# Kernel optimization log

Hardware: AMD Instinct MI355X
Metric: run time of the kernel (lower is better)

Reference implementation:

```python
import jax, jax.numpy as jnp
import numpy as np

N, L, H, D = 2, 4096, 12, 64
HD = H * D

def setup_inputs() -> dict:
    key = jax.random.key(0)
    ks = jax.random.split(key, 5)
    s = 1.0 / np.sqrt(HD)  # keep projections well-scaled
    return {
        "x": jax.random.normal(ks[0], (N, L, HD), dtype=jnp.float32),
        "Wq": jax.random.normal(ks[1], (HD, HD), dtype=jnp.float32) * s,
        "bq": jnp.zeros((HD,), dtype=jnp.float32),
        "Wk": jax.random.normal(ks[2], (HD, HD), dtype=jnp.float32) * s,
        "bk": jnp.zeros((HD,), dtype=jnp.float32),
        "Wv": jax.random.normal(ks[3], (HD, HD), dtype=jnp.float32) * s,
        "bv": jnp.zeros((HD,), dtype=jnp.float32),
        "Wo": jax.random.normal(ks[4], (HD, HD), dtype=jnp.float32) * s,
        "bo": jnp.zeros((HD,), dtype=jnp.float32),
        "train": 0,
    }

def reference(x, Wq, bq, Wk, bk, Wv, bv, Wo, bo, train):
    n, l, hd = x.shape
    h, d = H, D
    # QKV projections (hk.Linear: x @ W + b), reshape to (n, l, h, d)
    q = (x @ Wq + bq).reshape(n, l, h, d)
    k = (x @ Wk + bk).reshape(n, l, h, d)
    v = (x @ Wv + bv).reshape(n, l, h, d)
    # scores: (n, q, k, h), scaled by sqrt(key_size)
    qkt = jnp.einsum('nqhd,nkhd->nqkh', q, k) / jnp.sqrt(jnp.float32(d))
    attn = jax.nn.softmax(qkt, axis=2)
    # eval mode: dropout_rate is 0.0, so dropout is identity
    o = jnp.einsum('nqkh,nkhd->nqhd', attn, v).reshape(n, l, hd)
    return o @ Wo + bo
```

## Files before the change

### kernel.cpp

```cpp
#include <hip/hip_runtime.h>

#define NN 2
#define LL 4096
#define HH 12
#define DD 64
#define HD_ 768
#define M_TOT (NN * LL)

typedef __bf16 bf16_t;
typedef _Float16 f16_t;
typedef __bf16 bf16x8 __attribute__((ext_vector_type(8)));
typedef __bf16 bf16x4 __attribute__((ext_vector_type(4)));
typedef _Float16 f16x2 __attribute__((ext_vector_type(2)));
typedef _Float16 f16x4 __attribute__((ext_vector_type(4)));
typedef _Float16 f16x8 __attribute__((ext_vector_type(8)));
typedef float floatx4 __attribute__((ext_vector_type(4)));

#define QSCALE 0.1803368801111f

__device__ __forceinline__ void async_load16(const bf16_t* g, bf16_t* l) {
    __builtin_amdgcn_global_load_lds(
        (const __attribute__((address_space(1))) unsigned int*)(g),
        (__attribute__((address_space(3))) unsigned int*)(l),
        16, 0, 0);
}

__device__ __forceinline__ f16x2 pkrtz(float a, float b) {
    return __builtin_bit_cast(f16x2, __builtin_amdgcn_cvt_pkrtz(a, b));
}

__global__ void cvt_kernel(const float* __restrict__ src, bf16_t* __restrict__ dst, int n4) {
    int i = blockIdx.x * blockDim.x + threadIdx.x;
    if (i < n4) {
        const float4 v = ((const float4*)src)[i];
        bf16_t* d = dst + (size_t)i * 4;
        d[0] = (bf16_t)v.x; d[1] = (bf16_t)v.y; d[2] = (bf16_t)v.z; d[3] = (bf16_t)v.w;
    }
}

struct WtArgs { const float* W[4]; bf16_t* Wt[4]; };
__global__ void cvt_wt_kernel(WtArgs a) {
    const int z = blockIdx.z;
    int id = blockIdx.x * 256 + threadIdx.x;
    int k = id / HD_;
    int n = id % HD_;
    a.Wt[z][(size_t)n * HD_ + k] = (bf16_t)a.W[z][id];
}

__device__ __forceinline__ void gemm_tile64(
    const bf16_t* __restrict__ A, const bf16_t* __restrict__ Bt,
    bf16_t* As, bf16_t* Bs, int m0, int n0, floatx4 (&acc)[2][2])
{
    const int tid  = threadIdx.x;
    const int lane = tid & 63;
    const int quad = lane >> 4, l16 = lane & 15;
    const int wave = tid >> 6;
    const int wm = wave >> 1, wn = wave & 1;
    const int lrow = tid >> 2;
    const int lcol = (tid & 3) * 16;

    for (int kt = 0; kt < HD_; kt += 64) {
        __syncthreads();
        {
            const bf16_t* ga = A + (size_t)(m0 + lrow) * HD_ + kt + lcol;
            *(bf16x8*)&As[lrow * 72 + lcol]     = *(const bf16x8*)ga;
            *(bf16x8*)&As[lrow * 72 + lcol + 8] = *(const bf16x8*)(ga + 8);
            const bf16_t* gb = Bt + (size_t)(n0 + lrow) * HD_ + kt + lcol;
            *(bf16x8*)&Bs[lrow * 72 + lcol]     = *(const bf16x8*)gb;
            *(bf16x8*)&Bs[lrow * 72 + lcol + 8] = *(const bf16x8*)(gb + 8);
        }
        __syncthreads();
        for (int ks = 0; ks < 2; ++ks) {
            bf16x8 af[2], bfr[2];
            af[0]  = *(const bf16x8*)&As[(wm * 32 + l16) * 72 + ks * 32 + quad * 8];
            af[1]  = *(const bf16x8*)&As[(wm * 32 + 16 + l16) * 72 + ks * 32 + quad * 8];
            bfr[0] = *(const bf16x8*)&Bs[(wn * 32 + l16) * 72 + ks * 32 + quad * 8];
            bfr[1] = *(const bf16x8*)&Bs[(wn * 32 + 16 + l16) * 72 + ks * 32 + quad * 8];
            for (int mi = 0; mi < 2; ++mi)
                for (int ni = 0; ni < 2; ++ni)
                    acc[mi][ni] = __builtin_amdgcn_mfma_f32_16x16x32_bf16(
                        af[mi], bfr[ni], acc[mi][ni], 0, 0, 0);
        }
    }
}

struct QKVArgs {
    const bf16_t* Bt[3];
    const float* bias[3];
    void* out[3];
};
__global__ __launch_bounds__(256) void gemm_qkv_kernel(const bf16_t* __restrict__ A, QKVArgs p)
{
    __shared__ __align__(16) bf16_t As[64 * 72];
    __shared__ __align__(16) bf16_t Bs[64 * 72];
    const int z = blockIdx.z;
    const int m0 = blockIdx.y * 64, n0 = blockIdx.x * 64;

    floatx4 acc[2][2] = {};
    gemm_tile64(A, p.Bt[z], As, Bs, m0, n0, acc);

    const int tid  = threadIdx.x;
    const int lane = tid & 63;
    const int quad = lane >> 4, l16 = lane & 15;
    const int wave = tid >> 6;
    const int wm = wave >> 1, wn = wave & 1;
    const float scale = (z == 0) ? QSCALE : 1.0f;
    const float* bias = p.bias[z];

    for (int ni = 0; ni < 2; ++ni) {
        const int col = n0 + wn * 32 + ni * 16 + l16;
        const float bv = bias[col];
        const int h = col >> 6, d = col & 63;
        for (int mi = 0; mi < 2; ++mi) {
            for (int r = 0; r < 4; ++r) {
                const int row = m0 + wm * 32 + mi * 16 + quad * 4 + r;
                const float val = (acc[mi][ni][r] + bv) * scale;
                const int nn = row >> 12, l = row & 4095;
                if (z == 2)
                    ((f16_t*)p.out[2])[(((size_t)nn * HH + h) * DD + d) * LL + l] = (f16_t)val;
                else
                    ((bf16_t*)p.out[z])[(((size_t)nn * HH + h) * LL + l) * DD + d] = (bf16_t)val;
            }
        }
    }
}

__global__ __launch_bounds__(256) void gemm_o_kernel(
    const bf16_t* __restrict__ A, const bf16_t* __restrict__ Bt,
    const float* __restrict__ bias, float* __restrict__ Cout)
{
    __shared__ __align__(16) bf16_t As[64 * 72];
    __shared__ __align__(16) bf16_t Bs[64 * 72];
    const int m0 = blockIdx.y * 64, n0 = blockIdx.x * 64;

    floatx4 acc[2][2] = {};
    gemm_tile64(A, Bt, As, Bs, m0, n0, acc);

    const int tid  = threadIdx.x;
    const int lane = tid & 63;
    const int quad = lane >> 4, l16 = lane & 15;
    const int wave = tid >> 6;
    const int wm = wave >> 1, wn = wave & 1;

    for (int ni = 0; ni < 2; ++ni) {
        const int col = n0 + wn * 32 + ni * 16 + l16;
        const float bv = bias[col];
        for (int mi = 0; mi < 2; ++mi)
            for (int r = 0; r < 4; ++r) {
                const int row = m0 + wm * 32 + mi * 16 + quad * 4 + r;
                Cout[(size_t)row * HD_ + col] = acc[mi][ni][r] + bv;
            }
    }
}

__global__ __launch_bounds__(256) void attn_kernel(
    const bf16_t* __restrict__ qg, const bf16_t* __restrict__ kg,
    const f16_t* __restrict__ vtg, bf16_t* __restrict__ og)
{
    __shared__ union {
        struct {
            bf16_t Ks[8 * 64 * 8];
            f16_t  Va[16 * 64 * 4];
        } s;
        bf16_t OT[128 * 72];
    } u;

    const int tid  = threadIdx.x;
    const int w    = tid >> 6, lane = tid & 63;
    const int quad = lane >> 4, l16 = lane & 15;
    const int qt0  = blockIdx.x * 128;
    const int nh   = blockIdx.y;
    const int nIdx = nh / HH, hIdx = nh % HH;
    const size_t headL = (size_t)nh * LL;

    bf16x8 bq[2][2];
    for (int mi = 0; mi < 2; ++mi) {
        const int row = qt0 + w * 32 + mi * 16 + l16;
        const bf16_t* qp = qg + (headL + row) * DD + quad * 8;
        bq[mi][0] = *(const bf16x8*)qp;
        bq[mi][1] = *(const bf16x8*)(qp + 32);
    }

    const bf16_t* kptr = kg + (headL + w * 16 + l16) * DD + quad * 8;
    bf16_t* ldsK0 = &u.s.Ks[(0 * 4 + w) * 512];
    bf16_t* ldsK1 = &u.s.Ks[(1 * 4 + w) * 512];

    const int dsrc = tid >> 2, cch = tid & 3;
    const f16_t* vptr = vtg + ((size_t)nh * DD + dsrc) * LL + cch * 16;
    f16_t* vdst = &u.s.Va[((cch * 4 + (dsrc >> 4)) * 64 + (dsrc & 15)) * 4];

    floatx4 oacc[4][2] = {};
    float rowsum[2] = {0.f, 0.f};

    for (int t = 0; t < LL / 64; ++t) {
        f16x8 v0 = *(const f16x8*)vptr;
        f16x8 v1 = *(const f16x8*)(vptr + 8);
        vptr += 64;
        __syncthreads();
        async_load16(kptr,      ldsK0);
        async_load16(kptr + 32, ldsK1);
        kptr += 64 * DD;
        *(f16x4*)(vdst +   0) = __builtin_shufflevector(v0, v0, 0, 1, 2, 3);
        *(f16x4*)(vdst +  64) = __builtin_shufflevector(v0, v0, 4, 5, 6, 7);
        *(f16x4*)(vdst + 128) = __builtin_shufflevector(v1, v1, 0, 1, 2, 3);
        *(f16x4*)(vdst + 192) = __builtin_shufflevector(v1, v1, 4, 5, 6, 7);
        __syncthreads();

        floatx4 sacc[4][2] = {};
        for (int ks = 0; ks < 2; ++ks)
            for (int kb = 0; kb < 4; ++kb) {
                bf16x8 ak = *(const bf16x8*)&u.s.Ks[(ks * 4 + kb) * 512 + lane * 8];
                sacc[kb][0] = __builtin_amdgcn_mfma_f32_16x16x32_bf16(ak, bq[0][ks], sacc[kb][0], 0, 0, 0);
                sacc[kb][1] = __builtin_amdgcn_mfma_f32_16x16x32_bf16(ak, bq[1][ks], sacc[kb][1], 0, 0, 0);
            }

        f16x4 pf[4][2];
        for (int kb = 0; kb < 4; ++kb)
            for (int mi = 0; mi < 2; ++mi) {
                const float p0 = __builtin_amdgcn_exp2f(sacc[kb][mi][0]);
                const float p1 = __builtin_amdgcn_exp2f(sacc[kb][mi][1]);
                const float p2 = __builtin_amdgcn_exp2f(sacc[kb][mi][2]);
                const float p3 = __builtin_amdgcn_exp2f(sacc[kb][mi][3]);
                rowsum[mi] += (p0 + p1) + (p2 + p3);
                f16x2 lo = pkrtz(p0, p1);
                f16x2 hi = pkrtz(p2, p3);
                pf[kb][mi] = __builtin_shufflevector(lo, hi, 0, 1, 2, 3);
            }

        for (int kb = 0; kb < 4; ++kb)
            for (int db = 0; db < 4; ++db) {
                f16x4 av = *(const f16x4*)&u.s.Va[(kb * 4 + db) * 256 + lane * 4];
                oacc[db][0] = __builtin_amdgcn_mfma_f32_16x16x16f16(av, pf[kb][0], oacc[db][0], 0, 0, 0);
                oacc[db][1] = __builtin_amdgcn_mfma_f32_16x16x16f16(av, pf[kb][1], oacc[db][1], 0, 0, 0);
            }
    }

    float rinv[2];
    for (int mi = 0; mi < 2; ++mi) {
        float s = rowsum[mi];
        s += __shfl_xor(s, 16);
        s += __shfl_xor(s, 32);
        rinv[mi] = __builtin_amdgcn_rcpf(s);
    }

    __syncthreads();
    for (int db = 0; db < 4; ++db)
        for (int mi = 0; mi < 2; ++mi) {
            bf16x4 o4;
            for (int r = 0; r < 4; ++r)
                o4[r] = (bf16_t)(oacc[db][mi][r] * rinv[mi]);
            *(bf16x4*)&u.OT[(w * 32 + mi * 16 + l16) * 72 + db * 16 + quad * 4] = o4;
        }
    __syncthreads();

    const int q = tid >> 1, hf = tid & 1;
    const bf16_t* src = &u.OT[q * 72 + hf * 32];
    bf16x8 r0 = *(const bf16x8*)(src + 0);
    bf16x8 r1 = *(const bf16x8*)(src + 8);
    bf16x8 r2 = *(const bf16x8*)(src + 16);
    bf16x8 r3 = *(const bf16x8*)(src + 24);
    bf16_t* dst = og + ((size_t)nIdx * LL + qt0 + q) * HD_ + hIdx * 64 + hf * 32;
    *(bf16x8*)(dst + 0)  = r0;
    *(bf16x8*)(dst + 8)  = r1;
    *(bf16x8*)(dst + 16) = r2;
    *(bf16x8*)(dst + 24) = r3;
}

extern "C" void kernel_launch(void* const* d_in, const int* in_sizes, int n_in,
                              void* d_out, int out_size, void* d_ws, size_t ws_size,
                              hipStream_t stream) {
    const float* x  = (const float*)d_in[0];
    const float* Wq = (const float*)d_in[1];
    const float* bq = (const float*)d_in[2];
    const float* Wk = (const float*)d_in[3];
    const float* bk = (const float*)d_in[4];
    const float* Wv = (const float*)d_in[5];
    const float* bv = (const float*)d_in[6];
    const float* Wo = (const float*)d_in[7];
    const float* bo = (const float*)d_in[8];

    char* ws = (char*)d_ws;
    const size_t xbytes = (size_t)M_TOT * HD_ * 2;
    const size_t wbytes = (size_t)HD_ * HD_ * 2;

    bf16_t* xb  = (bf16_t*)ws; ws += xbytes;
    bf16_t* wqt = (bf16_t*)ws; ws += wbytes;
    bf16_t* wkt = (bf16_t*)ws; ws += wbytes;
    bf16_t* wvt = (bf16_t*)ws; ws += wbytes;
    bf16_t* wot = (bf16_t*)ws; ws += wbytes;
    bf16_t* qb  = (bf16_t*)ws; ws += xbytes;
    bf16_t* kb  = (bf16_t*)ws; ws += xbytes;
    f16_t*  vtb = (f16_t*)ws;  ws += xbytes;
    bf16_t* ob  = (bf16_t*)ws; ws += xbytes;

    cvt_kernel<<<(M_TOT * HD_ / 4 + 255) / 256, 256, 0, stream>>>(x, xb, M_TOT * HD_ / 4);

    WtArgs wa;
    wa.W[0] = Wq; wa.W[1] = Wk; wa.W[2] = Wv; wa.W[3] = Wo;
    wa.Wt[0] = wqt; wa.Wt[1] = wkt; wa.Wt[2] = wvt; wa.Wt[3] = wot;
    cvt_wt_kernel<<<dim3(HD_ * HD_ / 256, 1, 4), 256, 0, stream>>>(wa);

    QKVArgs qa;
    qa.Bt[0] = wqt; qa.Bt[1] = wkt; qa.Bt[2] = wvt;
    qa.bias[0] = bq; qa.bias[1] = bk; qa.bias[2] = bv;
    qa.out[0] = qb; qa.out[1] = kb; qa.out[2] = vtb;
    gemm_qkv_kernel<<<dim3(HD_ / 64, M_TOT / 64, 3), 256, 0, stream>>>(xb, qa);

    attn_kernel<<<dim3(LL / 128, NN * HH), 256, 0, stream>>>(qb, kb, vtb, ob);

    gemm_o_kernel<<<dim3(HD_ / 64, M_TOT / 64), 256, 0, stream>>>(ob, wot, bo, (float*)d_out);
}
```

Baseline: 366.4 us.

## Use 32x32 MFMA in attention with pre-swizzled K/V fragment layouts

The attention inner loop moves from 16x16 MFMA tiles to 32x32x16 bf16/f16 MFMA. The QKV GEMM epilogue now writes K and V straight into MFMA-fragment-ordered layouts, so the attention kernel can fill LDS with plain async global-to-LDS copies for both K and V, with no register staging or shuffling of V. The P matrix is rearranged between lane halves with xor-32 shuffles to form the f16 operand for the PV MFMA. This aims to cut LDS traffic and instruction overhead per tile, at the cost of scattered global stores in the projection epilogue and extra cross-lane shuffles.

```diff
diff --git a/kernel.cpp b/kernel.cpp
--- a/kernel.cpp
+++ b/kernel.cpp
@@ -6,6 +6,7 @@
 #define DD 64
 #define HD_ 768
 #define M_TOT (NN * LL)
+#define KVSTRIDE 262144
 
 typedef __bf16 bf16_t;
 typedef _Float16 f16_t;
@@ -15,10 +16,11 @@
 typedef _Float16 f16x4 __attribute__((ext_vector_type(4)));
 typedef _Float16 f16x8 __attribute__((ext_vector_type(8)));
 typedef float floatx4 __attribute__((ext_vector_type(4)));
+typedef float floatx16 __attribute__((ext_vector_type(16)));
 
 #define QSCALE 0.1803368801111f
 
-__device__ __forceinline__ void async_load16(const bf16_t* g, bf16_t* l) {
+__device__ __forceinline__ void async_load16(const void* g, void* l) {
     __builtin_amdgcn_global_load_lds(
         (const __attribute__((address_space(1))) unsigned int*)(g),
         (__attribute__((address_space(3))) unsigned int*)(l),
@@ -27,6 +29,13 @@
 
 __device__ __forceinline__ f16x2 pkrtz(float a, float b) {
     return __builtin_bit_cast(f16x2, __builtin_amdgcn_cvt_pkrtz(a, b));
+}
+
+__device__ __forceinline__ f16x4 shflx32(f16x4 v) {
+    int2 iv = __builtin_bit_cast(int2, v);
+    iv.x = __shfl_xor(iv.x, 32);
+    iv.y = __shfl_xor(iv.y, 32);
+    return __builtin_bit_cast(f16x4, iv);
 }
 
 __global__ void cvt_kernel(const float* __restrict__ src, bf16_t* __restrict__ dst, int n4) {
@@ -116,10 +125,18 @@
                 const int row = m0 + wm * 32 + mi * 16 + quad * 4 + r;
                 const float val = (acc[mi][ni][r] + bv) * scale;
                 const int nn = row >> 12, l = row & 4095;
-                if (z == 2)
-                    ((f16_t*)p.out[2])[(((size_t)nn * HH + h) * DD + d) * LL + l] = (f16_t)val;
-                else
-                    ((bf16_t*)p.out[z])[(((size_t)nn * HH + h) * LL + l) * DD + d] = (bf16_t)val;
+                const size_t nhb = (size_t)(nn * HH + h) * KVSTRIDE;
+                if (z == 0) {
+                    ((bf16_t*)p.out[0])[(((size_t)nn * HH + h) * LL + l) * DD + d] = (bf16_t)val;
+                } else if (z == 1) {
+                    size_t idx = nhb + (size_t)((l >> 5) * 4 + (d >> 4)) * 512
+                               + ((l & 31) + 32 * ((d >> 3) & 1)) * 8 + (d & 7);
+                    ((bf16_t*)p.out[1])[idx] = (bf16_t)val;
+                } else {
+                    size_t idx = nhb + (size_t)(((l >> 6) * 2 + (d >> 5)) * 4 + ((l >> 4) & 3)) * 512
+                               + ((d & 31) + 32 * ((l >> 3) & 1)) * 8 + (l & 7);
+                    ((f16_t*)p.out[2])[idx] = (f16_t)val;
+                }
             }
         }
     }
@@ -154,102 +171,89 @@
 }
 
 __global__ __launch_bounds__(256) void attn_kernel(
-    const bf16_t* __restrict__ qg, const bf16_t* __restrict__ kg,
-    const f16_t* __restrict__ vtg, bf16_t* __restrict__ og)
+    const bf16_t* __restrict__ qg, const bf16_t* __restrict__ kf,
+    const f16_t* __restrict__ vf, bf16_t* __restrict__ og)
 {
     __shared__ union {
         struct {
-            bf16_t Ks[8 * 64 * 8];
-            f16_t  Va[16 * 64 * 4];
+            bf16_t Ks[8 * 512];
+            f16_t  Vs[8 * 512];
         } s;
         bf16_t OT[128 * 72];
     } u;
 
-    const int tid  = threadIdx.x;
-    const int w    = tid >> 6, lane = tid & 63;
-    const int quad = lane >> 4, l16 = lane & 15;
-    const int qt0  = blockIdx.x * 128;
-    const int nh   = blockIdx.y;
+    const int tid = threadIdx.x;
+    const int w = tid >> 6, lane = tid & 63;
+    const int l32 = lane & 31, hi = lane >> 5;
+    const int qt0 = blockIdx.x * 128;
+    const int nh = blockIdx.y;
     const int nIdx = nh / HH, hIdx = nh % HH;
-    const size_t headL = (size_t)nh * LL;
-
-    bf16x8 bq[2][2];
-    for (int mi = 0; mi < 2; ++mi) {
-        const int row = qt0 + w * 32 + mi * 16 + l16;
-        const bf16_t* qp = qg + (headL + row) * DD + quad * 8;
-        bq[mi][0] = *(const bf16x8*)qp;
-        bq[mi][1] = *(const bf16x8*)(qp + 32);
-    }
-
-    const bf16_t* kptr = kg + (headL + w * 16 + l16) * DD + quad * 8;
-    bf16_t* ldsK0 = &u.s.Ks[(0 * 4 + w) * 512];
-    bf16_t* ldsK1 = &u.s.Ks[(1 * 4 + w) * 512];
-
-    const int dsrc = tid >> 2, cch = tid & 3;
-    const f16_t* vptr = vtg + ((size_t)nh * DD + dsrc) * LL + cch * 16;
-    f16_t* vdst = &u.s.Va[((cch * 4 + (dsrc >> 4)) * 64 + (dsrc & 15)) * 4];
-
-    floatx4 oacc[4][2] = {};
-    float rowsum[2] = {0.f, 0.f};
+
+    bf16x8 qfrag[4];
+    {
+        const bf16_t* qp = qg + ((size_t)nh * LL + qt0 + w * 32 + l32) * DD + hi * 8;
+        for (int s = 0; s < 4; ++s) qfrag[s] = *(const bf16x8*)(qp + s * 16);
+    }
+
+    const bf16_t* ksrc = kf + (size_t)nh * KVSTRIDE + (2 * w) * 512 + lane * 8;
+    const f16_t*  vsrc = vf + (size_t)nh * KVSTRIDE + (2 * w) * 512 + lane * 8;
+    bf16_t* kdst0 = &u.s.Ks[(2 * w) * 512 + lane * 8];
+    bf16_t* kdst1 = &u.s.Ks[(2 * w + 1) * 512 + lane * 8];
+    f16_t*  vdst0 = &u.s.Vs[(2 * w) * 512 + lane * 8];
+    f16_t*  vdst1 = &u.s.Vs[(2 * w + 1) * 512 + lane * 8];
+
+    floatx16 oacc[2] = {};
+    float rs = 0.f;
 
     for (int t = 0; t < LL / 64; ++t) {
-        f16x8 v0 = *(const f16x8*)vptr;
-        f16x8 v1 = *(const f16x8*)(vptr + 8);
-        vptr += 64;
         __syncthreads();
-        async_load16(kptr,      ldsK0);
-        async_load16(kptr + 32, ldsK1);
-        kptr += 64 * DD;
-        *(f16x4*)(vdst +   0) = __builtin_shufflevector(v0, v0, 0, 1, 2, 3);
-        *(f16x4*)(vdst +  64) = __builtin_shufflevector(v0, v0, 4, 5, 6, 7);
-        *(f16x4*)(vdst + 128) = __builtin_shufflevector(v1, v1, 0, 1, 2, 3);
-        *(f16x4*)(vdst + 192) = __builtin_shufflevector(v1, v1, 4, 5, 6, 7);
+        async_load16(ksrc, kdst0);
+        async_load16(ksrc + 512, kdst1);
+        async_load16(vsrc, vdst0);
+        async_load16(vsrc + 512, vdst1);
+        ksrc += 4096; vsrc += 4096;
         __syncthreads();
 
-        floatx4 sacc[4][2] = {};
-        for (int ks = 0; ks < 2; ++ks)
-            for (int kb = 0; kb < 4; ++kb) {
-                bf16x8 ak = *(const bf16x8*)&u.s.Ks[(ks * 4 + kb) * 512 + lane * 8];
-                sacc[kb][0] = __builtin_amdgcn_mfma_f32_16x16x32_bf16(ak, bq[0][ks], sacc[kb][0], 0, 0, 0);
-                sacc[kb][1] = __builtin_amdgcn_mfma_f32_16x16x32_bf16(ak, bq[1][ks], sacc[kb][1], 0, 0, 0);
+        for (int kvb = 0; kvb < 2; ++kvb) {
+            floatx16 sacc = {};
+            for (int s = 0; s < 4; ++s) {
+                bf16x8 ak = *(const bf16x8*)&u.s.Ks[(kvb * 4 + s) * 512 + lane * 8];
+                sacc = __builtin_amdgcn_mfma_f32_32x32x16_bf16(ak, qfrag[s], sacc, 0, 0, 0);
             }
-
-        f16x4 pf[4][2];
-        for (int kb = 0; kb < 4; ++kb)
-            for (int mi = 0; mi < 2; ++mi) {
-                const float p0 = __builtin_amdgcn_exp2f(sacc[kb][mi][0]);
-                const float p1 = __builtin_amdgcn_exp2f(sacc[kb][mi][1]);
-                const float p2 = __builtin_amdgcn_exp2f(sacc[kb][mi][2]);
-                const float p3 = __builtin_amdgcn_exp2f(sacc[kb][mi][3]);
-                rowsum[mi] += (p0 + p1) + (p2 + p3);
-                f16x2 lo = pkrtz(p0, p1);
-                f16x2 hi = pkrtz(p2, p3);
-                pf[kb][mi] = __builtin_shufflevector(lo, hi, 0, 1, 2, 3);
+            for (int sub = 0; sub < 2; ++sub) {
+                float p[8];
+                for (int i = 0; i < 8; ++i) {
+                    p[i] = __builtin_amdgcn_exp2f(sacc[sub * 8 + i]);
+                    rs += p[i];
+                }
+                f16x2 l01 = pkrtz(p[0], p[1]), l23 = pkrtz(p[2], p[3]);
+                f16x2 h45 = pkrtz(p[4], p[5]), h67 = pkrtz(p[6], p[7]);
+                f16x4 Lo = __builtin_shufflevector(l01, l23, 0, 1, 2, 3);
+                f16x4 Hh = __builtin_shufflevector(h45, h67, 0, 1, 2, 3);
+                f16x4 swL = shflx32(Lo);
+                f16x4 swH = shflx32(Hh);
+                f16x4 a03 = hi ? swH : Lo;
+                f16x4 a47 = hi ? Hh : swL;
+                f16x8 pf = __builtin_shufflevector(a03, a47, 0, 1, 2, 3, 4, 5, 6, 7);
+                const int kstep = kvb * 2 + sub;
+                for (int db = 0; db < 2; ++db) {
+                    f16x8 av = *(const f16x8*)&u.s.Vs[(db * 4 + kstep) * 512 + lane * 8];
+                    oacc[db] = __builtin_amdgcn_mfma_f32_32x32x16_f16(av, pf, oacc[db], 0, 0, 0);
+                }
             }
-
-        for (int kb = 0; kb < 4; ++kb)
-            for (int db = 0; db < 4; ++db) {
-                f16x4 av = *(const f16x4*)&u.s.Va[(kb * 4 + db) * 256 + lane * 4];
-                oacc[db][0] = __builtin_amdgcn_mfma_f32_16x16x16f16(av, pf[kb][0], oacc[db][0], 0, 0, 0);
-                oacc[db][1] = __builtin_amdgcn_mfma_f32_16x16x16f16(av, pf[kb][1], oacc[db][1], 0, 0, 0);
-            }
-    }
-
-    float rinv[2];
-    for (int mi = 0; mi < 2; ++mi) {
-        float s = rowsum[mi];
-        s += __shfl_xor(s, 16);
-        s += __shfl_xor(s, 32);
-        rinv[mi] = __builtin_amdgcn_rcpf(s);
-    }
+        }
+    }
+
+    rs += __shfl_xor(rs, 32);
+    const float rinv = __builtin_amdgcn_rcpf(rs);
 
     __syncthreads();
-    for (int db = 0; db < 4; ++db)
-        for (int mi = 0; mi < 2; ++mi) {
+    for (int db = 0; db < 2; ++db)
+        for (int g = 0; g < 4; ++g) {
             bf16x4 o4;
             for (int r = 0; r < 4; ++r)
-                o4[r] = (bf16_t)(oacc[db][mi][r] * rinv[mi]);
-            *(bf16x4*)&u.OT[(w * 32 + mi * 16 + l16) * 72 + db * 16 + quad * 4] = o4;
+                o4[r] = (bf16_t)(oacc[db][g * 4 + r] * rinv);
+            *(bf16x4*)&u.OT[(w * 32 + l32) * 72 + db * 32 + hi * 4 + g * 8] = o4;
         }
     __syncthreads();
 
@@ -289,8 +293,8 @@
     bf16_t* wvt = (bf16_t*)ws; ws += wbytes;
     bf16_t* wot = (bf16_t*)ws; ws += wbytes;
     bf16_t* qb  = (bf16_t*)ws; ws += xbytes;
-    bf16_t* kb  = (bf16_t*)ws; ws += xbytes;
-    f16_t*  vtb = (f16_t*)ws;  ws += xbytes;
+    bf16_t* kfb = (bf16_t*)ws; ws += xbytes;
+    f16_t*  vfb = (f16_t*)ws;  ws += xbytes;
     bf16_t* ob  = (bf16_t*)ws; ws += xbytes;
 
     cvt_kernel<<<(M_TOT * HD_ / 4 + 255) / 256, 256, 0, stream>>>(x, xb, M_TOT * HD_ / 4);
@@ -303,10 +307,10 @@
     QKVArgs qa;
     qa.Bt[0] = wqt; qa.Bt[1] = wkt; qa.Bt[2] = wvt;
     qa.bias[0] = bq; qa.bias[1] = bk; qa.bias[2] = bv;
-    qa.out[0] = qb; qa.out[1] = kb; qa.out[2] = vtb;
+    qa.out[0] = qb; qa.out[1] = kfb; qa.out[2] = vfb;
     gemm_qkv_kernel<<<dim3(HD_ / 64, M_TOT / 64, 3), 256, 0, stream>>>(xb, qa);
 
-    attn_kernel<<<dim3(LL / 128, NN * HH), 256, 0, stream>>>(qb, kb, vtb, ob);
+    attn_kernel<<<dim3(LL / 128, NN * HH), 256, 0, stream>>>(qb, kfb, vfb, ob);
 
     gemm_o_kernel<<<dim3(HD_ / 64, M_TOT / 64), 256, 0, stream>>>(ob, wot, bo, (float*)d_out);
 }
```

Result: faster. 353.3 us (-3.6%).
